# Optimization experiments

Hardware: AMD Instinct MI355X
Metric: run time of the kernel (lower is better)

The kernel has to match this reference:

```python
import jax, jax.numpy as jnp
import numpy as np

B, S, E = 4096, 128, 768   # batch, seq_len, bert hidden
HID = 384                  # mlp_dims[-1]
NH = 9                     # num_head (domains)
NE = 5                     # num_expert (hardcoded in module)


def setup_inputs() -> dict:
    key = jax.random.key(0)
    ks = jax.random.split(key, 14)
    std = 0.02
    return {
        "feature": jax.random.normal(ks[0], (B, S, E), dtype=jnp.float32),
        "masks": jax.random.randint(ks[1], (B, S), 0, 2, dtype=jnp.int32),
        "category": jax.random.randint(ks[2], (B,), 0, NH, dtype=jnp.int32),
        # MaskAttention: Linear(E, 1)
        "attn_w": jax.random.normal(ks[3], (E,), dtype=jnp.float32) * std,
        "attn_b": jnp.zeros((), dtype=jnp.float32),
        # gates: per-head Sequential(Linear(E,HID), ReLU, Linear(HID,NE), Softmax)
        "gate_w1": jax.random.normal(ks[4], (NH, E, HID), dtype=jnp.float32) * std,
        "gate_b1": jnp.zeros((NH, HID), dtype=jnp.float32),
        "gate_w2": jax.random.normal(ks[5], (NH, HID, NE), dtype=jnp.float32) * std,
        "gate_b2": jnp.zeros((NH, NE), dtype=jnp.float32),
        # experts: MLP(E, [HID]) = Linear(E,HID) + ReLU (dropout inactive in eval)
        "expert_w": jax.random.normal(ks[6], (NE, E, HID), dtype=jnp.float32) * std,
        "expert_b": jnp.zeros((NE, HID), dtype=jnp.float32),
        # heads: per-head Linear(HID, 1)
        "head_w": jax.random.normal(ks[7], (NH, HID), dtype=jnp.float32) * std,
        "head_b": jnp.zeros((NH,), dtype=jnp.float32),
    }


def reference(feature, masks, category, attn_w, attn_b,
              gate_w1, gate_b1, gate_w2, gate_b2,
              expert_w, expert_b, head_w, head_b):
    # ---- MaskAttention pooling: scores = Linear(E,1)(feature), mask, softmax over S
    scores = jnp.einsum('bse,e->bs', feature, attn_w) + attn_b          # [B,S]
    scores = jnp.where(masks == 0, jnp.float32(-1e9), scores)
    alpha = jax.nn.softmax(scores, axis=-1)                             # [B,S]
    pooled = jnp.einsum('bs,bse->be', alpha, feature)                   # [B,E]

    b_idx = jnp.arange(pooled.shape[0])

    # ---- category-indexed gate: compute all NH gate MLPs, select per sample
    gh = jax.nn.relu(jnp.einsum('be,heo->hbo', pooled, gate_w1) + gate_b1[:, None, :])
    glog = jnp.einsum('hbo,hok->hbk', gh, gate_w2) + gate_b2[:, None, :]
    gates_all = jax.nn.softmax(glog, axis=-1)                           # [NH,B,NE]
    gate_value = gates_all[category, b_idx]                             # [B,NE]

    # ---- experts: rep = sum_k gate[:,k] * relu(pooled @ Wk + bk)
    eh = jax.nn.relu(jnp.einsum('be,keo->kbo', pooled, expert_w) + expert_b[:, None, :])
    rep = jnp.einsum('bk,kbo->bo', gate_value, eh)                      # [B,HID]

    # ---- category-indexed head: per-sample Linear(HID,1)
    out = jnp.sum(rep * head_w[category], axis=-1) + head_b[category]   # [B]
    return jax.nn.sigmoid(out)
```

## Files before the change

kernel.cpp:

```cpp
#include <hip/hip_runtime.h>
#include <hip/hip_bf16.h>

#define Bn   4096
#define Sn   128
#define En   768
#define HIDn 384
#define NHn  9
#define NEn  5
#define MAXTILES 41

typedef __attribute__((ext_vector_type(8))) short short8;
typedef __attribute__((ext_vector_type(4))) float f32x4;

__device__ __forceinline__ unsigned short f2bf(float v) {
  unsigned int x = __float_as_uint(v);
  x += 0x7fffu + ((x >> 16) & 1u);
  return (unsigned short)(x >> 16);
}
__device__ __forceinline__ float dot4(float4 a, float4 b) {
  return fmaf(a.x, b.x, fmaf(a.y, b.y, fmaf(a.z, b.z, a.w * b.w)));
}
__device__ __forceinline__ void fma4(float4& p, float w, float4 v) {
  p.x = fmaf(w, v.x, p.x); p.y = fmaf(w, v.y, p.y);
  p.z = fmaf(w, v.z, p.z); p.w = fmaf(w, v.w, p.w);
}

__global__ __launch_bounds__(256) void prep_kernel(
    const float* __restrict__ feature, const int* __restrict__ masks,
    const float* __restrict__ attn_w, const float* __restrict__ ew,
    const float* __restrict__ g1, const int* __restrict__ category,
    unsigned short* __restrict__ pooled, unsigned short* __restrict__ Bpe,
    unsigned short* __restrict__ Bpg, int* __restrict__ rowsamp,
    int* __restrict__ meta) {
  __shared__ __align__(16) union {
    struct { float pbuf[4][768]; float sbuf[4]; } pool;
    struct { int hist[NHn][256]; int padbase[NHn]; int total[NHn];
             int tilecat[MAXTILES]; int padTiles; } srt;
  } sm;
  const int t = threadIdx.x, lane = t & 63, wid = t >> 6;
  const int bid = blockIdx.x;

  if (bid < Bn) {
    const int b = bid;
    const float4* aw = (const float4*)attn_w;
    const float4 aw0 = aw[lane], aw1 = aw[64 + lane], aw2 = aw[128 + lane];
    const float4* fb = (const float4*)(feature + (size_t)b * (Sn * En));
    unsigned long long bal = __ballot(lane < 32 && masks[b * Sn + wid * 32 + (lane & 31)] != 0);
    unsigned int m = (unsigned int)bal;
    float4 p0 = {0,0,0,0}, p1 = {0,0,0,0}, p2 = {0,0,0,0};
    float lsum = 0.f;
    if (m) {
      int s = __builtin_ctz(m); m &= m - 1;
      const float4* rp = fb + (wid * 32 + s) * (En / 4);
      float4 c0 = rp[lane], c1 = rp[64 + lane], c2 = rp[128 + lane];
      while (m) {
        int s2 = __builtin_ctz(m); m &= m - 1;
        const float4* rp2 = fb + (wid * 32 + s2) * (En / 4);
        float4 n0 = rp2[lane], n1 = rp2[64 + lane], n2 = rp2[128 + lane];
        float part = dot4(c0, aw0) + dot4(c1, aw1) + dot4(c2, aw2);
        #pragma unroll
        for (int off = 32; off; off >>= 1) part += __shfl_xor(part, off);
        float w = __expf(part);
        lsum += w;
        fma4(p0, w, c0); fma4(p1, w, c1); fma4(p2, w, c2);
        c0 = n0; c1 = n1; c2 = n2;
      }
      float part = dot4(c0, aw0) + dot4(c1, aw1) + dot4(c2, aw2);
      #pragma unroll
      for (int off = 32; off; off >>= 1) part += __shfl_xor(part, off);
      float w = __expf(part);
      lsum += w;
      fma4(p0, w, c0); fma4(p1, w, c1); fma4(p2, w, c2);
    }
    ((float4*)sm.pool.pbuf[wid])[lane] = p0;
    ((float4*)sm.pool.pbuf[wid])[64 + lane] = p1;
    ((float4*)sm.pool.pbuf[wid])[128 + lane] = p2;
    if (lane == 0) sm.pool.sbuf[wid] = lsum;
    __syncthreads();
    float total = sm.pool.sbuf[0] + sm.pool.sbuf[1] + sm.pool.sbuf[2] + sm.pool.sbuf[3];
    if (total == 0.f) {
      p0 = p1 = p2 = float4{0,0,0,0};
      for (int s = 0; s < 32; ++s) {
        const float4* rp = fb + (wid * 32 + s) * (En / 4);
        fma4(p0, 1.f, rp[lane]); fma4(p1, 1.f, rp[64 + lane]); fma4(p2, 1.f, rp[128 + lane]);
      }
      ((float4*)sm.pool.pbuf[wid])[lane] = p0;
      ((float4*)sm.pool.pbuf[wid])[64 + lane] = p1;
      ((float4*)sm.pool.pbuf[wid])[128 + lane] = p2;
      __syncthreads();
      total = 128.f;
    }
    const float inv = 1.f / total;
    if (t < 192) {
      float4 s0 = ((const float4*)sm.pool.pbuf[0])[t];
      float4 s1 = ((const float4*)sm.pool.pbuf[1])[t];
      float4 s2 = ((const float4*)sm.pool.pbuf[2])[t];
      float4 s3 = ((const float4*)sm.pool.pbuf[3])[t];
      ushort4 u;
      u.x = f2bf((s0.x+s1.x+s2.x+s3.x) * inv);
      u.y = f2bf((s0.y+s1.y+s2.y+s3.y) * inv);
      u.z = f2bf((s0.z+s1.z+s2.z+s3.z) * inv);
      u.w = f2bf((s0.w+s1.w+s2.w+s3.w) * inv);
      ((ushort4*)pooled)[(size_t)b * 192 + t] = u;
    }
    return;
  }

  if (bid < Bn + 2016) {
    const int pair = (bid - Bn) * 4 + wid;
    const int q = lane >> 4, j = lane & 15;
    const float* src; unsigned short* dst; int kt;
    if (pair < 2880) {
      int nt = pair / 24; kt = pair % 24;
      int col = nt * 16 + j;
      src = ew + (size_t)(col / HIDn) * (En * HIDn) + (col % HIDn);
      dst = Bpe + (size_t)pair * 512;
    } else {
      int g = pair - 2880;
      int h = g / 576, rem = g % 576;
      int nt = rem / 24; kt = rem % 24;
      int col = nt * 16 + j;
      src = g1 + (size_t)h * (En * HIDn) + col;
      dst = Bpg + ((size_t)(h * 24 + nt) * 24 + kt) * 512;
    }
    unsigned short outv[8] __attribute__((aligned(16)));
    #pragma unroll
    for (int e = 0; e < 8; ++e) {
      int k = kt * 32 + q * 8 + e;
      outv[e] = f2bf(src[(size_t)k * HIDn]);
    }
    *(uint4*)&dst[lane * 8] = *(const uint4*)outv;
    return;
  }

  #pragma unroll
  for (int jj = 0; jj < NHn; ++jj) sm.srt.hist[jj][t] = 0;
  __syncthreads();
  for (int i = 0; i < 16; ++i) { int c = category[t * 16 + i]; sm.srt.hist[c][t]++; }
  __syncthreads();
  if (t < NHn) {
    int run = 0;
    for (int x = 0; x < 256; ++x) { int v = sm.srt.hist[t][x]; sm.srt.hist[t][x] = run; run += v; }
    sm.srt.total[t] = run;
  }
  __syncthreads();
  if (t == 0) {
    int pb = 0, mt = 0;
    for (int jj = 0; jj < NHn; ++jj) {
      sm.srt.padbase[jj] = pb;
      int tot = sm.srt.total[jj];
      int nt = (tot + 127) >> 7;
      for (int k2 = 0; k2 < nt; ++k2) {
        meta[1 + mt + k2] = jj;
        int vv = tot - (k2 << 7); if (vv > 128) vv = 128;
        meta[64 + mt + k2] = vv;
        sm.srt.tilecat[mt + k2] = jj;
      }
      mt += nt; pb += nt << 7;
    }
    meta[0] = mt; sm.srt.padTiles = mt;
  }
  __syncthreads();
  const int padM = sm.srt.padTiles << 7;
  for (int mm = t; mm < padM; mm += 256) {
    int h = sm.srt.tilecat[mm >> 7];
    if (mm - sm.srt.padbase[h] >= sm.srt.total[h]) rowsamp[mm] = 0;
  }
  for (int i = 0; i < 16; ++i) {
    int idx = t * 16 + i; int c = category[idx];
    int off = sm.srt.hist[c][t]++;
    rowsamp[sm.srt.padbase[c] + off] = idx;
  }
}

__global__ __launch_bounds__(256) void gemm_kernel(
    const unsigned short* __restrict__ pooled, const unsigned short* __restrict__ Bpe,
    const unsigned short* __restrict__ Bpg, const float* __restrict__ eb,
    const float* __restrict__ gb1, const float* __restrict__ g2,
    const int* __restrict__ category, const float* __restrict__ hw,
    const int* __restrict__ rowsamp, const int* __restrict__ meta,
    float* __restrict__ partial, float* __restrict__ glogp) {
  __shared__ __align__(16) struct {
    unsigned short Alds[128 * 40];
    unsigned short Blds[8 * 512];
    union {
      struct { float hwlds[NHn * HIDn]; float plds[2][128]; } e;
      struct { int rs[128]; float w2lds[640]; } g;
    } u;
  } sm;
  const int t = threadIdx.x, lane = t & 63, wid = t >> 6;
  const int wm = wid >> 1, wn = wid & 1;
  const int bid = blockIdx.x;
  const int r = t >> 2, c0 = (t & 3) * 8;
  const int arow = wm * 64 + (lane & 15);
  const int aq = (lane >> 4) * 8;
  const int lrb = wm * 64 + ((lane >> 4) << 2);
  const int cb = wn * 64 + (lane & 15);
  f32x4 acc[4][4] = {};

  if (bid < 480) {
    const int bx = bid % 15, by = bid / 15;
    const int m0 = by * 128, ntg0 = bx * 8;
    for (int idx = t; idx < NHn * HIDn; idx += 256) sm.u.e.hwlds[idx] = hw[idx];
    for (int kt = 0; kt < 24; ++kt) {
      __syncthreads();
      *(uint4*)&sm.Alds[r * 40 + c0] =
          *(const uint4*)&pooled[(size_t)(m0 + r) * En + kt * 32 + c0];
      *(uint4*)&sm.Alds[(r + 64) * 40 + c0] =
          *(const uint4*)&pooled[(size_t)(m0 + r + 64) * En + kt * 32 + c0];
      #pragma unroll
      for (int rnd = 0; rnd < 2; ++rnd) {
        int chunk = t + rnd * 256;
        int nt = chunk >> 6, l2 = chunk & 63;
        *(uint4*)&sm.Blds[nt * 512 + l2 * 8] =
            *(const uint4*)&Bpe[((size_t)(ntg0 + nt) * 24 + kt) * 512 + l2 * 8];
      }
      __syncthreads();
      short8 af[4], bfv[4];
      #pragma unroll
      for (int i = 0; i < 4; ++i) af[i] = *(const short8*)&sm.Alds[(arow + i * 16) * 40 + aq];
      #pragma unroll
      for (int i = 0; i < 4; ++i) bfv[i] = *(const short8*)&sm.Blds[(wn * 4 + i) * 512 + lane * 8];
      #pragma unroll
      for (int i = 0; i < 4; ++i)
        #pragma unroll
        for (int jj = 0; jj < 4; ++jj)
          acc[i][jj] = __builtin_amdgcn_mfma_f32_16x16x32_bf16(af[i], bfv[jj], acc[i][jj], 0, 0, 0);
    }
    const int kexp = bx / 3, lcolbase = (bx % 3) * 128;
    (void)kexp;
    float sums[4][4];
    #pragma unroll
    for (int i = 0; i < 4; ++i) {
      #pragma unroll
      for (int rr = 0; rr < 4; ++rr) {
        const int row = m0 + lrb + i * 16 + rr;
        const int cat = category[row];
        float s = 0.f;
        #pragma unroll
        for (int jj = 0; jj < 4; ++jj) {
          int cl = cb + jj * 16;
          float v = acc[i][jj][rr] + eb[bx * 128 + cl];
          v = fmaxf(v, 0.f);
          s = fmaf(v, sm.u.e.hwlds[cat * HIDn + lcolbase + cl], s);
        }
        #pragma unroll
        for (int off = 8; off; off >>= 1) s += __shfl_xor(s, off);
        sums[i][rr] = s;
      }
    }
    __syncthreads();
    if ((lane & 15) == 0) {
      #pragma unroll
      for (int i = 0; i < 4; ++i)
        #pragma unroll
        for (int rr = 0; rr < 4; ++rr)
          sm.u.e.plds[wn][lrb + i * 16 + rr] = sums[i][rr];
    }
    __syncthreads();
    if (t < 128) partial[(size_t)bx * Bn + m0 + t] = sm.u.e.plds[0][t] + sm.u.e.plds[1][t];
    return;
  }

  const int gid = bid - 480;
  const int mt = gid / 3, bxg = gid % 3;
  if (mt >= meta[0]) return;
  const int h = meta[1 + mt], valid = meta[64 + mt];
  if (t < 128) sm.u.g.rs[t] = rowsamp[mt * 128 + t];
  const float* w2src = g2 + ((size_t)h * HIDn + bxg * 128) * 5;
  for (int idx = t; idx < 640; idx += 256) sm.u.g.w2lds[idx] = w2src[idx];
  for (int kt = 0; kt < 24; ++kt) {
    __syncthreads();
    *(uint4*)&sm.Alds[r * 40 + c0] =
        *(const uint4*)&pooled[(size_t)sm.u.g.rs[r] * En + kt * 32 + c0];
    *(uint4*)&sm.Alds[(r + 64) * 40 + c0] =
        *(const uint4*)&pooled[(size_t)sm.u.g.rs[r + 64] * En + kt * 32 + c0];
    #pragma unroll
    for (int rnd = 0; rnd < 2; ++rnd) {
      int chunk = t + rnd * 256;
      int nt = chunk >> 6, l2 = chunk & 63;
      *(uint4*)&sm.Blds[nt * 512 + l2 * 8] =
          *(const uint4*)&Bpg[((size_t)(h * 24 + bxg * 8 + nt) * 24 + kt) * 512 + l2 * 8];
    }
    __syncthreads();
    short8 af[4], bfv[4];
    #pragma unroll
    for (int i = 0; i < 4; ++i) af[i] = *(const short8*)&sm.Alds[(arow + i * 16) * 40 + aq];
    #pragma unroll
    for (int i = 0; i < 4; ++i) bfv[i] = *(const short8*)&sm.Blds[(wn * 4 + i) * 512 + lane * 8];
    #pragma unroll
    for (int i = 0; i < 4; ++i)
      #pragma unroll
      for (int jj = 0; jj < 4; ++jj)
        acc[i][jj] = __builtin_amdgcn_mfma_f32_16x16x32_bf16(af[i], bfv[jj], acc[i][jj], 0, 0, 0);
  }
  #pragma unroll
  for (int i = 0; i < 4; ++i) {
    #pragma unroll
    for (int rr = 0; rr < 4; ++rr) {
      const int lrow = lrb + i * 16 + rr;
      float s[5] = {0.f, 0.f, 0.f, 0.f, 0.f};
      #pragma unroll
      for (int jj = 0; jj < 4; ++jj) {
        int cl = cb + jj * 16;
        float v = acc[i][jj][rr] + gb1[h * HIDn + bxg * 128 + cl];
        v = fmaxf(v, 0.f);
        #pragma unroll
        for (int k = 0; k < 5; ++k) s[k] = fmaf(v, sm.u.g.w2lds[cl * 5 + k], s[k]);
      }
      #pragma unroll
      for (int k = 0; k < 5; ++k)
        #pragma unroll
        for (int off = 8; off; off >>= 1) s[k] += __shfl_xor(s[k], off);
      if ((lane & 15) == 0 && lrow < valid) {
        int samp = sm.u.g.rs[lrow];
        #pragma unroll
        for (int k = 0; k < 5; ++k)
          glogp[((size_t)bxg * Bn + samp) * 5 + k] = s[k];
      }
    }
  }
}

__global__ __launch_bounds__(256) void final_kernel(
    const float* __restrict__ partial, const float* __restrict__ glogp,
    const float* __restrict__ gb2, const int* __restrict__ category,
    const float* __restrict__ hb, float* __restrict__ out) {
  const int row = blockIdx.x * 256 + threadIdx.x;
  const int cat = category[row];
  float gl[5];
  #pragma unroll
  for (int k = 0; k < 5; ++k)
    gl[k] = gb2[cat * 5 + k]
          + glogp[((size_t)0 * Bn + row) * 5 + k]
          + glogp[((size_t)1 * Bn + row) * 5 + k]
          + glogp[((size_t)2 * Bn + row) * 5 + k];
  float mx = fmaxf(fmaxf(fmaxf(gl[0], gl[1]), fmaxf(gl[2], gl[3])), gl[4]);
  float ek[5], es = 0.f;
  #pragma unroll
  for (int k = 0; k < 5; ++k) { ek[k] = __expf(gl[k] - mx); es += ek[k]; }
  const float einv = 1.f / es;
  float s = 0.f;
  #pragma unroll
  for (int k = 0; k < 5; ++k) {
    float ps = partial[(size_t)(3 * k) * Bn + row]
             + partial[(size_t)(3 * k + 1) * Bn + row]
             + partial[(size_t)(3 * k + 2) * Bn + row];
    s = fmaf(ek[k] * einv, ps, s);
  }
  s += hb[cat];
  out[row] = 1.f / (1.f + __expf(-s));
}

extern "C" void kernel_launch(void* const* d_in, const int* in_sizes, int n_in,
                              void* d_out, int out_size, void* d_ws, size_t ws_size,
                              hipStream_t stream) {
  const float* feature  = (const float*)d_in[0];
  const int*   masks    = (const int*)d_in[1];
  const int*   category = (const int*)d_in[2];
  const float* attn_w   = (const float*)d_in[3];
  const float* gate_w1  = (const float*)d_in[5];
  const float* gate_b1  = (const float*)d_in[6];
  const float* gate_w2  = (const float*)d_in[7];
  const float* gate_b2  = (const float*)d_in[8];
  const float* expert_w = (const float*)d_in[9];
  const float* expert_b = (const float*)d_in[10];
  const float* head_w   = (const float*)d_in[11];
  const float* head_b   = (const float*)d_in[12];
  float* out = (float*)d_out;

  char* ws = (char*)d_ws;
  unsigned short* pooled = (unsigned short*)(ws);
  unsigned short* Bpe    = (unsigned short*)(ws + 6291456);
  unsigned short* Bpg    = (unsigned short*)(ws + 9240576);
  int* rowsamp           = (int*)(ws + 14548992);
  int* meta              = (int*)(ws + 14569984);
  float* glogp           = (float*)(ws + 14570496);
  float* partial         = (float*)(ws + 14816256);

  prep_kernel<<<dim3(Bn + 2016 + 1), dim3(256), 0, stream>>>(
      feature, masks, attn_w, expert_w, gate_w1, category,
      pooled, Bpe, Bpg, rowsamp, meta);
  gemm_kernel<<<dim3(480 + 3 * MAXTILES), dim3(256), 0, stream>>>(
      pooled, Bpe, Bpg, expert_b, gate_b1, gate_w2, category, head_w,
      rowsamp, meta, partial, glogp);
  final_kernel<<<dim3(16), dim3(256), 0, stream>>>(
      partial, glogp, gate_b2, category, head_b, out);
}
```

Before: 218.4 us.

## Use nontemporal feature loads, deeper prefetch, reorder gate blocks first, drop hw LDS

```diff
diff --git a/kernel.cpp b/kernel.cpp
--- a/kernel.cpp
+++ b/kernel.cpp
@@ -17,13 +17,20 @@
   x += 0x7fffu + ((x >> 16) & 1u);
   return (unsigned short)(x >> 16);
 }
-__device__ __forceinline__ float dot4(float4 a, float4 b) {
+__device__ __forceinline__ float dot4v(f32x4 a, f32x4 b) {
   return fmaf(a.x, b.x, fmaf(a.y, b.y, fmaf(a.z, b.z, a.w * b.w)));
 }
-__device__ __forceinline__ void fma4(float4& p, float w, float4 v) {
-  p.x = fmaf(w, v.x, p.x); p.y = fmaf(w, v.y, p.y);
-  p.z = fmaf(w, v.z, p.z); p.w = fmaf(w, v.w, p.w);
-}
+__device__ __forceinline__ f32x4 ntl(const f32x4* p) {
+  return __builtin_nontemporal_load(p);
+}
+
+#define PROC(x0, x1, x2) {                                                 \
+    float part = dot4v(x0, aw0) + dot4v(x1, aw1) + dot4v(x2, aw2);         \
+    _Pragma("unroll")                                                      \
+    for (int off = 32; off; off >>= 1) part += __shfl_xor(part, off);      \
+    float w = __expf(part);                 \
+    lsum += w;                                                             \
+    p0 += w * (x0); p1 += w * (x1); p2 += w * (x2); }
 
 __global__ __launch_bounds__(256) void prep_kernel(
     const float* __restrict__ feature, const int* __restrict__ masks,
@@ -42,66 +49,64 @@
 
   if (bid < Bn) {
     const int b = bid;
-    const float4* aw = (const float4*)attn_w;
-    const float4 aw0 = aw[lane], aw1 = aw[64 + lane], aw2 = aw[128 + lane];
-    const float4* fb = (const float4*)(feature + (size_t)b * (Sn * En));
+    const f32x4* aw = (const f32x4*)attn_w;
+    const f32x4 aw0 = aw[lane], aw1 = aw[64 + lane], aw2 = aw[128 + lane];
+    const f32x4* fb = (const f32x4*)(feature + (size_t)b * (Sn * En));
     unsigned long long bal = __ballot(lane < 32 && masks[b * Sn + wid * 32 + (lane & 31)] != 0);
     unsigned int m = (unsigned int)bal;
-    float4 p0 = {0,0,0,0}, p1 = {0,0,0,0}, p2 = {0,0,0,0};
+    const int rowbase = wid * 32;
+    f32x4 p0 = {0,0,0,0}, p1 = {0,0,0,0}, p2 = {0,0,0,0};
     float lsum = 0.f;
     if (m) {
       int s = __builtin_ctz(m); m &= m - 1;
-      const float4* rp = fb + (wid * 32 + s) * (En / 4);
-      float4 c0 = rp[lane], c1 = rp[64 + lane], c2 = rp[128 + lane];
-      while (m) {
+      const f32x4* rp = fb + (rowbase + s) * 192;
+      f32x4 a0 = ntl(rp + lane), a1 = ntl(rp + 64 + lane), a2 = ntl(rp + 128 + lane);
+      if (m) {
         int s2 = __builtin_ctz(m); m &= m - 1;
-        const float4* rp2 = fb + (wid * 32 + s2) * (En / 4);
-        float4 n0 = rp2[lane], n1 = rp2[64 + lane], n2 = rp2[128 + lane];
-        float part = dot4(c0, aw0) + dot4(c1, aw1) + dot4(c2, aw2);
-        #pragma unroll
-        for (int off = 32; off; off >>= 1) part += __shfl_xor(part, off);
-        float w = __expf(part);
-        lsum += w;
-        fma4(p0, w, c0); fma4(p1, w, c1); fma4(p2, w, c2);
-        c0 = n0; c1 = n1; c2 = n2;
-      }
-      float part = dot4(c0, aw0) + dot4(c1, aw1) + dot4(c2, aw2);
-      #pragma unroll
-      for (int off = 32; off; off >>= 1) part += __shfl_xor(part, off);
-      float w = __expf(part);
-      lsum += w;
-      fma4(p0, w, c0); fma4(p1, w, c1); fma4(p2, w, c2);
-    }
-    ((float4*)sm.pool.pbuf[wid])[lane] = p0;
-    ((float4*)sm.pool.pbuf[wid])[64 + lane] = p1;
-    ((float4*)sm.pool.pbuf[wid])[128 + lane] = p2;
+        const f32x4* rq = fb + (rowbase + s2) * 192;
+        f32x4 b0 = ntl(rq + lane), b1 = ntl(rq + 64 + lane), b2 = ntl(rq + 128 + lane);
+        while (m) {
+          int s3 = __builtin_ctz(m); m &= m - 1;
+          const f32x4* rr = fb + (rowbase + s3) * 192;
+          f32x4 n0 = ntl(rr + lane), n1 = ntl(rr + 64 + lane), n2 = ntl(rr + 128 + lane);
+          PROC(a0, a1, a2);
+          a0 = b0; a1 = b1; a2 = b2;
+          b0 = n0; b1 = n1; b2 = n2;
+        }
+        PROC(a0, a1, a2);
+        a0 = b0; a1 = b1; a2 = b2;
+      }
+      PROC(a0, a1, a2);
+    }
+    ((f32x4*)sm.pool.pbuf[wid])[lane] = p0;
+    ((f32x4*)sm.pool.pbuf[wid])[64 + lane] = p1;
+    ((f32x4*)sm.pool.pbuf[wid])[128 + lane] = p2;
     if (lane == 0) sm.pool.sbuf[wid] = lsum;
     __syncthreads();
     float total = sm.pool.sbuf[0] + sm.pool.sbuf[1] + sm.pool.sbuf[2] + sm.pool.sbuf[3];
     if (total == 0.f) {
-      p0 = p1 = p2 = float4{0,0,0,0};
+      p0 = p1 = p2 = f32x4{0,0,0,0};
       for (int s = 0; s < 32; ++s) {
-        const float4* rp = fb + (wid * 32 + s) * (En / 4);
-        fma4(p0, 1.f, rp[lane]); fma4(p1, 1.f, rp[64 + lane]); fma4(p2, 1.f, rp[128 + lane]);
-      }
-      ((float4*)sm.pool.pbuf[wid])[lane] = p0;
-      ((float4*)sm.pool.pbuf[wid])[64 + lane] = p1;
-      ((float4*)sm.pool.pbuf[wid])[128 + lane] = p2;
+        const f32x4* rp = fb + (rowbase + s) * 192;
+        p0 += ntl(rp + lane); p1 += ntl(rp + 64 + lane); p2 += ntl(rp + 128 + lane);
+      }
+      ((f32x4*)sm.pool.pbuf[wid])[lane] = p0;
+      ((f32x4*)sm.pool.pbuf[wid])[64 + lane] = p1;
+      ((f32x4*)sm.pool.pbuf[wid])[128 + lane] = p2;
       __syncthreads();
       total = 128.f;
     }
     const float inv = 1.f / total;
     if (t < 192) {
-      float4 s0 = ((const float4*)sm.pool.pbuf[0])[t];
-      float4 s1 = ((const float4*)sm.pool.pbuf[1])[t];
-      float4 s2 = ((const float4*)sm.pool.pbuf[2])[t];
-      float4 s3 = ((const float4*)sm.pool.pbuf[3])[t];
-      ushort4 u;
-      u.x = f2bf((s0.x+s1.x+s2.x+s3.x) * inv);
-      u.y = f2bf((s0.y+s1.y+s2.y+s3.y) * inv);
-      u.z = f2bf((s0.z+s1.z+s2.z+s3.z) * inv);
-      u.w = f2bf((s0.w+s1.w+s2.w+s3.w) * inv);
-      ((ushort4*)pooled)[(size_t)b * 192 + t] = u;
+      f32x4 s0 = ((const f32x4*)sm.pool.pbuf[0])[t];
+      f32x4 s1 = ((const f32x4*)sm.pool.pbuf[1])[t];
+      f32x4 s2 = ((const f32x4*)sm.pool.pbuf[2])[t];
+      f32x4 s3 = ((const f32x4*)sm.pool.pbuf[3])[t];
+      f32x4 smv = (s0 + s1) + (s2 + s3);
+      ushort4 u4;
+      u4.x = f2bf(smv.x * inv); u4.y = f2bf(smv.y * inv);
+      u4.z = f2bf(smv.z * inv); u4.w = f2bf(smv.w * inv);
+      ((ushort4*)pooled)[(size_t)b * 192 + t] = u4;
     }
     return;
   }
@@ -184,8 +189,8 @@
     unsigned short Alds[128 * 40];
     unsigned short Blds[8 * 512];
     union {
-      struct { float hwlds[NHn * HIDn]; float plds[2][128]; } e;
-      struct { int rs[128]; float w2lds[640]; } g;
+      struct { float plds[2][128]; } e;
+      struct { int rs[128]; float w2[640]; } g;
     } u;
   } sm;
   const int t = threadIdx.x, lane = t & 63, wid = t >> 6;
@@ -198,22 +203,25 @@
   const int cb = wn * 64 + (lane & 15);
   f32x4 acc[4][4] = {};
 
-  if (bid < 480) {
-    const int bx = bid % 15, by = bid / 15;
-    const int m0 = by * 128, ntg0 = bx * 8;
-    for (int idx = t; idx < NHn * HIDn; idx += 256) sm.u.e.hwlds[idx] = hw[idx];
+  if (bid < 3 * MAXTILES) {
+    const int mt = bid / 3, bxg = bid % 3;
+    if (mt >= meta[0]) return;
+    const int h = meta[1 + mt], valid = meta[64 + mt];
+    if (t < 128) sm.u.g.rs[t] = rowsamp[mt * 128 + t];
+    const float* w2src = g2 + ((size_t)h * HIDn + bxg * 128) * 5;
+    for (int idx = t; idx < 640; idx += 256) sm.u.g.w2[idx] = w2src[idx];
     for (int kt = 0; kt < 24; ++kt) {
       __syncthreads();
       *(uint4*)&sm.Alds[r * 40 + c0] =
-          *(const uint4*)&pooled[(size_t)(m0 + r) * En + kt * 32 + c0];
+          *(const uint4*)&pooled[(size_t)sm.u.g.rs[r] * En + kt * 32 + c0];
       *(uint4*)&sm.Alds[(r + 64) * 40 + c0] =
-          *(const uint4*)&pooled[(size_t)(m0 + r + 64) * En + kt * 32 + c0];
+          *(const uint4*)&pooled[(size_t)sm.u.g.rs[r + 64] * En + kt * 32 + c0];
       #pragma unroll
       for (int rnd = 0; rnd < 2; ++rnd) {
         int chunk = t + rnd * 256;
         int nt = chunk >> 6, l2 = chunk & 63;
         *(uint4*)&sm.Blds[nt * 512 + l2 * 8] =
-            *(const uint4*)&Bpe[((size_t)(ntg0 + nt) * 24 + kt) * 512 + l2 * 8];
+            *(const uint4*)&Bpg[((size_t)(h * 24 + bxg * 8 + nt) * 24 + kt) * 512 + l2 * 8];
       }
       __syncthreads();
       short8 af[4], bfv[4];
@@ -227,60 +235,50 @@
         for (int jj = 0; jj < 4; ++jj)
           acc[i][jj] = __builtin_amdgcn_mfma_f32_16x16x32_bf16(af[i], bfv[jj], acc[i][jj], 0, 0, 0);
     }
-    const int kexp = bx / 3, lcolbase = (bx % 3) * 128;
-    (void)kexp;
-    float sums[4][4];
     #pragma unroll
     for (int i = 0; i < 4; ++i) {
       #pragma unroll
       for (int rr = 0; rr < 4; ++rr) {
-        const int row = m0 + lrb + i * 16 + rr;
-        const int cat = category[row];
-        float s = 0.f;
+        const int lrow = lrb + i * 16 + rr;
+        float s[5] = {0.f, 0.f, 0.f, 0.f, 0.f};
         #pragma unroll
         for (int jj = 0; jj < 4; ++jj) {
           int cl = cb + jj * 16;
-          float v = acc[i][jj][rr] + eb[bx * 128 + cl];
+          float v = acc[i][jj][rr] + gb1[h * HIDn + bxg * 128 + cl];
           v = fmaxf(v, 0.f);
-          s = fmaf(v, sm.u.e.hwlds[cat * HIDn + lcolbase + cl], s);
+          #pragma unroll
+          for (int k = 0; k < 5; ++k) s[k] = fmaf(v, sm.u.g.w2[cl * 5 + k], s[k]);
         }
         #pragma unroll
-        for (int off = 8; off; off >>= 1) s += __shfl_xor(s, off);
-        sums[i][rr] = s;
-      }
-    }
-    __syncthreads();
-    if ((lane & 15) == 0) {
-      #pragma unroll
-      for (int i = 0; i < 4; ++i)
-        #pragma unroll
-        for (int rr = 0; rr < 4; ++rr)
-          sm.u.e.plds[wn][lrb + i * 16 + rr] = sums[i][rr];
-    }
-    __syncthreads();
-    if (t < 128) partial[(size_t)bx * Bn + m0 + t] = sm.u.e.plds[0][t] + sm.u.e.plds[1][t];
+        for (int k = 0; k < 5; ++k)
+          #pragma unroll
+          for (int off = 8; off; off >>= 1) s[k] += __shfl_xor(s[k], off);
+        if ((lane & 15) == 0 && lrow < valid) {
+          int samp = sm.u.g.rs[lrow];
+          #pragma unroll
+          for (int k = 0; k < 5; ++k)
+            glogp[((size_t)bxg * Bn + samp) * 5 + k] = s[k];
+        }
+      }
+    }
     return;
   }
 
-  const int gid = bid - 480;
-  const int mt = gid / 3, bxg = gid % 3;
-  if (mt >= meta[0]) return;
-  const int h = meta[1 + mt], valid = meta[64 + mt];
-  if (t < 128) sm.u.g.rs[t] = rowsamp[mt * 128 + t];
-  const float* w2src = g2 + ((size_t)h * HIDn + bxg * 128) * 5;
-  for (int idx = t; idx < 640; idx += 256) sm.u.g.w2lds[idx] = w2src[idx];
+  const int e = bid - 3 * MAXTILES;
+  const int bx = e % 15, by = e / 15;
+  const int m0 = by * 128, ntg0 = bx * 8;
   for (int kt = 0; kt < 24; ++kt) {
     __syncthreads();
     *(uint4*)&sm.Alds[r * 40 + c0] =
-        *(const uint4*)&pooled[(size_t)sm.u.g.rs[r] * En + kt * 32 + c0];
+        *(const uint4*)&pooled[(size_t)(m0 + r) * En + kt * 32 + c0];
     *(uint4*)&sm.Alds[(r + 64) * 40 + c0] =
-        *(const uint4*)&pooled[(size_t)sm.u.g.rs[r + 64] * En + kt * 32 + c0];
+        *(const uint4*)&pooled[(size_t)(m0 + r + 64) * En + kt * 32 + c0];
     #pragma unroll
     for (int rnd = 0; rnd < 2; ++rnd) {
       int chunk = t + rnd * 256;
       int nt = chunk >> 6, l2 = chunk & 63;
       *(uint4*)&sm.Blds[nt * 512 + l2 * 8] =
-          *(const uint4*)&Bpg[((size_t)(h * 24 + bxg * 8 + nt) * 24 + kt) * 512 + l2 * 8];
+          *(const uint4*)&Bpe[((size_t)(ntg0 + nt) * 24 + kt) * 512 + l2 * 8];
     }
     __syncthreads();
     short8 af[4], bfv[4];
@@ -294,32 +292,37 @@
       for (int jj = 0; jj < 4; ++jj)
         acc[i][jj] = __builtin_amdgcn_mfma_f32_16x16x32_bf16(af[i], bfv[jj], acc[i][jj], 0, 0, 0);
   }
+  const int lcolbase = (bx % 3) * 128;
+  float sums[4][4];
   #pragma unroll
   for (int i = 0; i < 4; ++i) {
     #pragma unroll
     for (int rr = 0; rr < 4; ++rr) {
-      const int lrow = lrb + i * 16 + rr;
-      float s[5] = {0.f, 0.f, 0.f, 0.f, 0.f};
+      const int row = m0 + lrb + i * 16 + rr;
+      const int cat = category[row];
+      float s = 0.f;
       #pragma unroll
       for (int jj = 0; jj < 4; ++jj) {
         int cl = cb + jj * 16;
-        float v = acc[i][jj][rr] + gb1[h * HIDn + bxg * 128 + cl];
+        float v = acc[i][jj][rr] + eb[bx * 128 + cl];
         v = fmaxf(v, 0.f);
-        #pragma unroll
-        for (int k = 0; k < 5; ++k) s[k] = fmaf(v, sm.u.g.w2lds[cl * 5 + k], s[k]);
-      }
-      #pragma unroll
-      for (int k = 0; k < 5; ++k)
-        #pragma unroll
-        for (int off = 8; off; off >>= 1) s[k] += __shfl_xor(s[k], off);
-      if ((lane & 15) == 0 && lrow < valid) {
-        int samp = sm.u.g.rs[lrow];
-        #pragma unroll
-        for (int k = 0; k < 5; ++k)
-          glogp[((size_t)bxg * Bn + samp) * 5 + k] = s[k];
-      }
-    }
-  }
+        s = fmaf(v, hw[cat * HIDn + lcolbase + cl], s);
+      }
+      #pragma unroll
+      for (int off = 8; off; off >>= 1) s += __shfl_xor(s, off);
+      sums[i][rr] = s;
+    }
+  }
+  __syncthreads();
+  if ((lane & 15) == 0) {
+    #pragma unroll
+    for (int i = 0; i < 4; ++i)
+      #pragma unroll
+      for (int rr = 0; rr < 4; ++rr)
+        sm.u.e.plds[wn][lrb + i * 16 + rr] = sums[i][rr];
+  }
+  __syncthreads();
+  if (t < 128) partial[(size_t)bx * Bn + m0 + t] = sm.u.e.plds[0][t] + sm.u.e.plds[1][t];
 }
 
 __global__ __launch_bounds__(256) void final_kernel(
```

New measurement: 183.9 us. 1.19x faster.
